# Performance work log

Measured on AMD Instinct MI355X. Metric: run time of the kernel, lower is better.

Reference implementation:

```python
import jax, jax.numpy as jnp
import numpy as np

HEADS = 16
HEAD_DIM = 64
EMBED = HEADS * HEAD_DIM  # 1024
N, L = 4, 4096


def setup_inputs() -> dict:
    key = jax.random.key(0)
    k1, k2, k3, k4, k5, k6, k7, k8 = jax.random.split(key, 8)
    s = 0.02
    return {
        "q": jax.random.normal(k1, (N, L, EMBED), jnp.float32),
        "k": jax.random.normal(k2, (N, L, EMBED), jnp.float32),
        "v": jax.random.normal(k3, (N, L, EMBED), jnp.float32),
        "mask": jnp.ones((N, L, HEADS, HEADS), jnp.int32),
        # torch Linear weights: (out_features, in_features)
        "q_w": jax.random.normal(k4, (HEAD_DIM, HEAD_DIM), jnp.float32) * s,
        "k_w": jax.random.normal(k5, (HEAD_DIM, HEAD_DIM), jnp.float32) * s,
        "v_w": jax.random.normal(k6, (HEAD_DIM, HEAD_DIM), jnp.float32) * s,
        "fc_w": jax.random.normal(k7, (EMBED, EMBED), jnp.float32) * s,
        "fc_b": jax.random.normal(k8, (EMBED,), jnp.float32) * s,
    }


def reference(q, k, v, mask, q_w, k_w, v_w, fc_w, fc_b):
    n, ql = q.shape[0], q.shape[1]
    # reshape to (N, L, H, D) and apply per-head-dim linear projections (x @ W.T)
    q4 = q.reshape(n, ql, HEADS, HEAD_DIM) @ q_w.T
    k4 = k.reshape(n, k.shape[1], HEADS, HEAD_DIM) @ k_w.T
    v4 = v.reshape(n, v.shape[1], HEADS, HEAD_DIM) @ v_w.T
    # Faithful to the original: matmul broadcasts over (N, L), contracting head_dim,
    # so logits are (N, L, H, H) -- attention across heads per token.
    scale = 1.0 / jnp.sqrt(jnp.float32(HEAD_DIM))
    logits = jnp.einsum("nlhd,nlgd->nlhg", q4, k4) * scale
    logits = jnp.where(mask == 0, -jnp.inf, logits)
    weights = jax.nn.softmax(logits, axis=-1)
    out4 = jnp.einsum("nlhg,nlgd->nlhd", weights, v4)  # (N, L, H, D)
    # Faithful scrambled reshape: permute to (N, H, L, D) then flatten to (N, L, H*D)
    out = out4.transpose(0, 2, 1, 3).reshape(n, ql, HEADS * HEAD_DIM)
    return out @ fc_w.T + fc_b
```

## Files before the change

### kernel.cpp

```cpp
#include <hip/hip_runtime.h>
#include <hip/hip_bf16.h>
#include <stdint.h>

#define TOKENS 16384
#define LSEQ 4096
#define WPAD 72
#define NT 4

typedef short bf16x8 __attribute__((ext_vector_type(8)));
typedef float f32x4 __attribute__((ext_vector_type(4)));

typedef __attribute__((address_space(1))) void as1_t;
typedef __attribute__((address_space(3))) void as3_t;

__device__ __forceinline__ unsigned short f2bf(float x) {
  __hip_bfloat16 t = __float2bfloat16(x);
  return *reinterpret_cast<unsigned short*>(&t);
}

__device__ __forceinline__ bf16x8 pack8(float4 a, float4 b) {
  bf16x8 t;
  t[0] = (short)f2bf(a.x); t[1] = (short)f2bf(a.y);
  t[2] = (short)f2bf(a.z); t[3] = (short)f2bf(a.w);
  t[4] = (short)f2bf(b.x); t[5] = (short)f2bf(b.y);
  t[6] = (short)f2bf(b.z); t[7] = (short)f2bf(b.w);
  return t;
}

__device__ __forceinline__ void async16(const void* g, void* lds) {
  __builtin_amdgcn_global_load_lds((as1_t*)const_cast<void*>(g),
                                   (as3_t*)lds, 16, 0, 0);
}

__device__ __forceinline__ float4 aload(const float* p) {
  float4 r;
  asm volatile("global_load_dwordx4 %0, %1, off" : "=v"(r) : "v"(p));
  return r;
}
__device__ __forceinline__ int4 aloadi(const int* p) {
  int4 r;
  asm volatile("global_load_dwordx4 %0, %1, off" : "=v"(r) : "v"(p));
  return r;
}
#define WAITCNT(n) asm volatile("s_waitcnt vmcnt(" #n ")" ::: "memory")
#define SBAR() __builtin_amdgcn_sched_barrier(0)

__global__ __launch_bounds__(256) void cvt_bf16(const float* __restrict__ s,
                                                unsigned short* __restrict__ d,
                                                int n4) {
  int i = blockIdx.x * 256 + threadIdx.x;
  if (i < n4) {
    float4 f = ((const float4*)s)[i];
    union { unsigned short us[4]; uint2 u2; } pk;
    pk.us[0] = f2bf(f.x); pk.us[1] = f2bf(f.y);
    pk.us[2] = f2bf(f.z); pk.us[3] = f2bf(f.w);
    ((uint2*)d)[i] = pk.u2;
  }
}

__global__ __launch_bounds__(1024) void prep_weights(
    const float* __restrict__ qw, const float* __restrict__ kw,
    const float* __restrict__ vw, unsigned short* __restrict__ Mout,
    unsigned short* __restrict__ vwout) {
  __shared__ float ql[4096], kl[4096];
  const int t = threadIdx.x;
  ((float4*)ql)[t] = ((const float4*)qw)[t];
  ((float4*)kl)[t] = ((const float4*)kw)[t];
  {
    float4 f = ((const float4*)vw)[t];
    union { unsigned short us[4]; uint2 u2; } pk;
    pk.us[0] = f2bf(f.x); pk.us[1] = f2bf(f.y);
    pk.us[2] = f2bf(f.z); pk.us[3] = f2bf(f.w);
    ((uint2*)vwout)[t] = pk.u2;
  }
  __syncthreads();
  const int f = t >> 4;
  const int e0 = (t & 15) * 4;
  float acc0 = 0.f, acc1 = 0.f, acc2 = 0.f, acc3 = 0.f;
#pragma unroll 8
  for (int d = 0; d < 64; ++d) {
    const float qv = ql[d * 64 + f];
    const float4 kv = *(const float4*)&kl[d * 64 + e0];
    acc0 += qv * kv.x; acc1 += qv * kv.y; acc2 += qv * kv.z; acc3 += qv * kv.w;
  }
  union { unsigned short us[4]; uint2 u2; } pk;
  pk.us[0] = f2bf(acc0); pk.us[1] = f2bf(acc1);
  pk.us[2] = f2bf(acc2); pk.us[3] = f2bf(acc3);
  *(uint2*)&Mout[f * 64 + e0] = pk.u2;
}

__global__ __launch_bounds__(256) void attn8(
    const float* __restrict__ q, const float* __restrict__ k,
    const float* __restrict__ v, const int* __restrict__ mask,
    const unsigned short* __restrict__ Mg, const unsigned short* __restrict__ vwg,
    unsigned short* __restrict__ X) {
  __shared__ char Mlb[8192];
  __shared__ char Vwb[8192];
  __shared__ char scr_[4][2048];

  const int tid = threadIdx.x;
  const int l = tid & 63, w = tid >> 6;
  const int lr = l & 15, lg = l >> 4;
  char* scr = scr_[w];

#pragma unroll
  for (int i = 0; i < 2; ++i) {
    const int idx = tid + i * 256;
    const int row = idx >> 3, c = idx & 7;
    const int dst = row * 128 + ((c * 16) ^ ((row & 7) << 4));
    *(uint4*)(Mlb + dst) = *(const uint4*)(Mg + row * 64 + c * 8);
    *(uint4*)(Vwb + dst) = *(const uint4*)(vwg + row * 64 + c * 8);
  }
  __syncthreads();

  const int r7 = lr & 7;
  const int wc0 = (lg * 16) ^ (r7 << 4);
  const int wc1 = (64 + lg * 16) ^ (r7 << 4);
  const int fr0 = lr * 128 + ((lg * 16) ^ (r7 << 4));
  const int fr1 = lr * 128 + ((64 + lg * 16) ^ (r7 << 4));
  const int off = lr * 64 + lg * 8;

  const int tok0 = (blockIdx.x * 4 + w) * NT;

  float4 L[12];
  int4 Lm;
  {
    const size_t tb = (size_t)tok0 * 1024;
    L[0] = aload(q + tb + off);      L[1] = aload(q + tb + off + 4);
    L[2] = aload(q + tb + off + 32); L[3] = aload(q + tb + off + 36);
    L[4] = aload(k + tb + off);      L[5] = aload(k + tb + off + 4);
    L[6] = aload(k + tb + off + 32); L[7] = aload(k + tb + off + 36);
    L[8] = aload(v + tb + off);      L[9] = aload(v + tb + off + 4);
    L[10] = aload(v + tb + off + 32); L[11] = aload(v + tb + off + 36);
    Lm = aloadi(mask + (size_t)tok0 * 256 + lr * 16 + lg * 4);
  }

#pragma unroll
  for (int t = 0; t < NT; ++t) {
    const int tok = tok0 + t;

    if (t == 0) { WAITCNT(0); } else { WAITCNT(2); }
    SBAR();

    const bf16x8 aq0 = pack8(L[0], L[1]),  aq1 = pack8(L[2], L[3]);
    const bf16x8 ak0 = pack8(L[4], L[5]),  ak1 = pack8(L[6], L[7]);
    const bf16x8 av0 = pack8(L[8], L[9]),  av1 = pack8(L[10], L[11]);
    const int4 mk4 = Lm;
    SBAR();

    if (t < NT - 1) {
      const size_t tb = (size_t)(tok + 1) * 1024;
      L[0] = aload(q + tb + off);      L[1] = aload(q + tb + off + 4);
      L[2] = aload(q + tb + off + 32); L[3] = aload(q + tb + off + 36);
      L[4] = aload(k + tb + off);      L[5] = aload(k + tb + off + 4);
      L[6] = aload(k + tb + off + 32); L[7] = aload(k + tb + off + 36);
      L[8] = aload(v + tb + off);      L[9] = aload(v + tb + off + 4);
      L[10] = aload(v + tb + off + 32); L[11] = aload(v + tb + off + 36);
      Lm = aloadi(mask + (size_t)(tok + 1) * 256 + lr * 16 + lg * 4);
    }
    SBAR();

    f32x4 accu[4], accv[4];
#pragma unroll
    for (int n = 0; n < 4; ++n) {
      const int wrow = (n * 16 + lr) * 128;
      f32x4 z = {};
      const bf16x8 bm0 = *(const bf16x8*)(Mlb + wrow + wc0);
      const bf16x8 bm1 = *(const bf16x8*)(Mlb + wrow + wc1);
      accu[n] = __builtin_amdgcn_mfma_f32_16x16x32_bf16(ak0, bm0, z, 0, 0, 0);
      accu[n] = __builtin_amdgcn_mfma_f32_16x16x32_bf16(ak1, bm1, accu[n], 0, 0, 0);
      const bf16x8 bw0 = *(const bf16x8*)(Vwb + wrow + wc0);
      const bf16x8 bw1 = *(const bf16x8*)(Vwb + wrow + wc1);
      accv[n] = __builtin_amdgcn_mfma_f32_16x16x32_bf16(av0, bw0, z, 0, 0, 0);
      accv[n] = __builtin_amdgcn_mfma_f32_16x16x32_bf16(av1, bw1, accv[n], 0, 0, 0);
    }

#pragma unroll
    for (int n = 0; n < 4; ++n)
#pragma unroll
      for (int r = 0; r < 4; ++r) {
        const int row = lg * 4 + r;
        *(unsigned short*)(scr + row * 128 + ((32 * n + 2 * lr) ^ ((row & 7) << 4))) =
            f2bf(accu[n][r]);
      }
    const bf16x8 ua0 = *(const bf16x8*)(scr + fr0);
    const bf16x8 ua1 = *(const bf16x8*)(scr + fr1);
    f32x4 z4 = {};
    f32x4 st = __builtin_amdgcn_mfma_f32_16x16x32_bf16(ua0, aq0, z4, 0, 0, 0);
    st = __builtin_amdgcn_mfma_f32_16x16x32_bf16(ua1, aq1, st, 0, 0, 0);

    float e[4];
    float sm = 0.f;
    const int mks[4] = {mk4.x, mk4.y, mk4.z, mk4.w};
#pragma unroll
    for (int r = 0; r < 4; ++r) {
      e[r] = (mks[r] != 0) ? __expf(st[r] * 0.125f) : 0.f;
      sm += e[r];
    }
    sm += __shfl_xor(sm, 16);
    sm += __shfl_xor(sm, 32);
    const float inv = 1.0f / sm;
#pragma unroll
    for (int r = 0; r < 4; ++r) e[r] *= inv;

    bf16x8 apv;
#pragma unroll
    for (int j = 0; j < 8; ++j) {
      const int srcg = (lg * 2 + (j >> 2)) & 3;
      const float pv = __shfl(e[j & 3], lr + srcg * 16, 64);
      apv[j] = (short)((lg < 2) ? f2bf(pv) : (unsigned short)0);
    }

    const int s0 = lr + ((lg & 1) * 2) * 16;
    const int s1 = s0 + 16;
    f32x4 o[4];
#pragma unroll
    for (int n = 0; n < 4; ++n) {
      bf16x8 bv;
#pragma unroll
      for (int j = 0; j < 8; ++j) {
        const float xv = __shfl(accv[n][j & 3], (j < 4) ? s0 : s1, 64);
        bv[j] = (short)f2bf(xv);
      }
      f32x4 z = {};
      o[n] = __builtin_amdgcn_mfma_f32_16x16x32_bf16(apv, bv, z, 0, 0, 0);
    }

#pragma unroll
    for (int n = 0; n < 4; ++n)
#pragma unroll
      for (int r = 0; r < 4; ++r) {
        const int row = lg * 4 + r;
        *(unsigned short*)(scr + row * 128 + ((32 * n + 2 * lr) ^ ((row & 7) << 4))) =
            f2bf(o[n][r]);
      }
    const int nb = tok >> 12, lpos = tok & (LSEQ - 1);
#pragma unroll
    for (int it = 0; it < 2; ++it) {
      const int idx = it * 64 + l;
      const int h = idx >> 3, c = idx & 7;
      const uint4 val = *(const uint4*)(scr + h * 128 + ((c * 16) ^ ((h & 7) << 4)));
      *(uint4*)&X[((size_t)(nb * 16 + h) * LSEQ + lpos) * 64 + c * 8] = val;
    }
  }
}

__global__ __launch_bounds__(256) void gemm_fc(const unsigned short* __restrict__ A,
                                               const unsigned short* __restrict__ B,
                                               const float* __restrict__ bias,
                                               float* __restrict__ C) {
  __shared__ unsigned short sA[128 * 32];
  __shared__ unsigned short sB[128 * 32];
  const int tid = threadIdx.x;
  const int l = tid & 63, w = tid >> 6;
  const int wr = w >> 1, wc = w & 1;

  const int bid = blockIdx.x;
  const int wg = (bid & 7) * 128 + (bid >> 3);
  const int tm = (wg >> 3) * 128;
  const int tn = (wg & 7) * 128;

  f32x4 acc[4][4] = {};

  const int r0 = w * 16 + (l >> 2);
  const int c8 = (l & 3) * 8;

  for (int kt = 0; kt < 32; ++kt) {
    const int k0 = kt * 32;
#pragma unroll
    for (int s = 0; s < 2; ++s) {
      async16(A + (size_t)(tm + s * 64 + r0) * 1024 + k0 + c8,
              (char*)sA + s * 4096 + w * 1024);
      async16(B + (size_t)(tn + s * 64 + r0) * 1024 + k0 + c8,
              (char*)sB + s * 4096 + w * 1024);
    }
    __syncthreads();

    bf16x8 af[4], bfr[4];
#pragma unroll
    for (int fi = 0; fi < 4; ++fi)
      af[fi] = *(const bf16x8*)((const char*)sA +
                                (wr * 64 + fi * 16 + (l & 15)) * 64 + (l >> 4) * 16);
#pragma unroll
    for (int fj = 0; fj < 4; ++fj)
      bfr[fj] = *(const bf16x8*)((const char*)sB +
                                 (wc * 64 + fj * 16 + (l & 15)) * 64 + (l >> 4) * 16);
#pragma unroll
    for (int fi = 0; fi < 4; ++fi)
#pragma unroll
      for (int fj = 0; fj < 4; ++fj)
        acc[fi][fj] = __builtin_amdgcn_mfma_f32_16x16x32_bf16(af[fi], bfr[fj],
                                                              acc[fi][fj], 0, 0, 0);
    __syncthreads();
  }

#pragma unroll
  for (int fj = 0; fj < 4; ++fj) {
    const int col = tn + wc * 64 + fj * 16 + (l & 15);
    const float bv = bias[col];
#pragma unroll
    for (int fi = 0; fi < 4; ++fi) {
#pragma unroll
      for (int r = 0; r < 4; ++r) {
        const int row = tm + wr * 64 + fi * 16 + (l >> 4) * 4 + r;
        C[(size_t)row * 1024 + col] = acc[fi][fj][r] + bv;
      }
    }
  }
}

extern "C" void kernel_launch(void* const* d_in, const int* in_sizes, int n_in,
                              void* d_out, int out_size, void* d_ws, size_t ws_size,
                              hipStream_t stream) {
  (void)in_sizes; (void)n_in; (void)out_size; (void)ws_size;
  const float* q   = (const float*)d_in[0];
  const float* k   = (const float*)d_in[1];
  const float* v   = (const float*)d_in[2];
  const int*  mask = (const int*)d_in[3];
  const float* qw  = (const float*)d_in[4];
  const float* kw  = (const float*)d_in[5];
  const float* vw  = (const float*)d_in[6];
  const float* fcw = (const float*)d_in[7];
  const float* fcb = (const float*)d_in[8];
  float* out = (float*)d_out;

  unsigned short* X   = (unsigned short*)d_ws;
  unsigned short* Wb  = X + (size_t)16 * 1024 * 1024;
  unsigned short* Mw  = Wb + (size_t)1024 * 1024;
  unsigned short* vwb = Mw + 4096;

  cvt_bf16<<<dim3(1024), dim3(256), 0, stream>>>(fcw, Wb, 262144);
  prep_weights<<<dim3(1), dim3(1024), 0, stream>>>(qw, kw, vw, Mw, vwb);
  attn8<<<dim3(1024), dim3(256), 0, stream>>>(q, k, v, mask, Mw, vwb, X);
  gemm_fc<<<dim3(1024), dim3(256), 0, stream>>>(X, Wb, fcb, out);
}
```

Before: 116.1 us.

## Process one token per wave with direct weight loads and LDS V transpose

```diff
diff --git a/kernel.cpp b/kernel.cpp
--- a/kernel.cpp
+++ b/kernel.cpp
@@ -4,8 +4,7 @@
 
 #define TOKENS 16384
 #define LSEQ 4096
-#define WPAD 72
-#define NT 4
+#define VPAD 24
 
 typedef short bf16x8 __attribute__((ext_vector_type(8)));
 typedef float f32x4 __attribute__((ext_vector_type(4)));
@@ -89,159 +88,115 @@
   *(uint2*)&Mout[f * 64 + e0] = pk.u2;
 }
 
-__global__ __launch_bounds__(256) void attn8(
+__global__ __launch_bounds__(256) void attn9(
     const float* __restrict__ q, const float* __restrict__ k,
     const float* __restrict__ v, const int* __restrict__ mask,
     const unsigned short* __restrict__ Mg, const unsigned short* __restrict__ vwg,
     unsigned short* __restrict__ X) {
-  __shared__ char Mlb[8192];
-  __shared__ char Vwb[8192];
   __shared__ char scr_[4][2048];
+  __shared__ unsigned short vt_[4][64 * VPAD];
 
   const int tid = threadIdx.x;
   const int l = tid & 63, w = tid >> 6;
   const int lr = l & 15, lg = l >> 4;
   char* scr = scr_[w];
-
-#pragma unroll
-  for (int i = 0; i < 2; ++i) {
-    const int idx = tid + i * 256;
-    const int row = idx >> 3, c = idx & 7;
-    const int dst = row * 128 + ((c * 16) ^ ((row & 7) << 4));
-    *(uint4*)(Mlb + dst) = *(const uint4*)(Mg + row * 64 + c * 8);
-    *(uint4*)(Vwb + dst) = *(const uint4*)(vwg + row * 64 + c * 8);
-  }
-  __syncthreads();
+  unsigned short* VT = vt_[w];
+
+  const int tok = blockIdx.x * 4 + w;
+  const size_t tb = (size_t)tok * 1024;
+  const int off = lr * 64 + lg * 8;
+
+  float4 L0 = aload(q + tb + off),      L1 = aload(q + tb + off + 4);
+  float4 L2 = aload(q + tb + off + 32), L3 = aload(q + tb + off + 36);
+  float4 L4 = aload(k + tb + off),      L5 = aload(k + tb + off + 4);
+  float4 L6 = aload(k + tb + off + 32), L7 = aload(k + tb + off + 36);
+  float4 L8 = aload(v + tb + off),      L9 = aload(v + tb + off + 4);
+  float4 La = aload(v + tb + off + 32), Lb = aload(v + tb + off + 36);
+  int4 mk4 = aloadi(mask + (size_t)tok * 256 + lr * 16 + lg * 4);
+  WAITCNT(0);
+  SBAR();
+
+  const bf16x8 aq0 = pack8(L0, L1), aq1 = pack8(L2, L3);
+  const bf16x8 ak0 = pack8(L4, L5), ak1 = pack8(L6, L7);
+  const bf16x8 av0 = pack8(L8, L9), av1 = pack8(La, Lb);
+
+  f32x4 accu[4], accv[4];
+#pragma unroll
+  for (int n = 0; n < 4; ++n) {
+    const int wrow = (n * 16 + lr) * 64;
+    f32x4 z = {};
+    const bf16x8 bm0 = *(const bf16x8*)(Mg + wrow + lg * 8);
+    const bf16x8 bm1 = *(const bf16x8*)(Mg + wrow + 32 + lg * 8);
+    accu[n] = __builtin_amdgcn_mfma_f32_16x16x32_bf16(ak0, bm0, z, 0, 0, 0);
+    accu[n] = __builtin_amdgcn_mfma_f32_16x16x32_bf16(ak1, bm1, accu[n], 0, 0, 0);
+    const bf16x8 bw0 = *(const bf16x8*)(vwg + wrow + lg * 8);
+    const bf16x8 bw1 = *(const bf16x8*)(vwg + wrow + 32 + lg * 8);
+    accv[n] = __builtin_amdgcn_mfma_f32_16x16x32_bf16(av0, bw0, z, 0, 0, 0);
+    accv[n] = __builtin_amdgcn_mfma_f32_16x16x32_bf16(av1, bw1, accv[n], 0, 0, 0);
+  }
+
+#pragma unroll
+  for (int n = 0; n < 4; ++n)
+#pragma unroll
+    for (int r = 0; r < 4; ++r) {
+      const int row = lg * 4 + r;
+      *(unsigned short*)(scr + row * 128 + ((32 * n + 2 * lr) ^ ((row & 7) << 4))) =
+          f2bf(accu[n][r]);
+      VT[(n * 16 + lr) * VPAD + lg * 4 + r] = f2bf(accv[n][r]);
+    }
 
   const int r7 = lr & 7;
-  const int wc0 = (lg * 16) ^ (r7 << 4);
-  const int wc1 = (64 + lg * 16) ^ (r7 << 4);
-  const int fr0 = lr * 128 + ((lg * 16) ^ (r7 << 4));
-  const int fr1 = lr * 128 + ((64 + lg * 16) ^ (r7 << 4));
-  const int off = lr * 64 + lg * 8;
-
-  const int tok0 = (blockIdx.x * 4 + w) * NT;
-
-  float4 L[12];
-  int4 Lm;
-  {
-    const size_t tb = (size_t)tok0 * 1024;
-    L[0] = aload(q + tb + off);      L[1] = aload(q + tb + off + 4);
-    L[2] = aload(q + tb + off + 32); L[3] = aload(q + tb + off + 36);
-    L[4] = aload(k + tb + off);      L[5] = aload(k + tb + off + 4);
-    L[6] = aload(k + tb + off + 32); L[7] = aload(k + tb + off + 36);
-    L[8] = aload(v + tb + off);      L[9] = aload(v + tb + off + 4);
-    L[10] = aload(v + tb + off + 32); L[11] = aload(v + tb + off + 36);
-    Lm = aloadi(mask + (size_t)tok0 * 256 + lr * 16 + lg * 4);
-  }
-
-#pragma unroll
-  for (int t = 0; t < NT; ++t) {
-    const int tok = tok0 + t;
-
-    if (t == 0) { WAITCNT(0); } else { WAITCNT(2); }
-    SBAR();
-
-    const bf16x8 aq0 = pack8(L[0], L[1]),  aq1 = pack8(L[2], L[3]);
-    const bf16x8 ak0 = pack8(L[4], L[5]),  ak1 = pack8(L[6], L[7]);
-    const bf16x8 av0 = pack8(L[8], L[9]),  av1 = pack8(L[10], L[11]);
-    const int4 mk4 = Lm;
-    SBAR();
-
-    if (t < NT - 1) {
-      const size_t tb = (size_t)(tok + 1) * 1024;
-      L[0] = aload(q + tb + off);      L[1] = aload(q + tb + off + 4);
-      L[2] = aload(q + tb + off + 32); L[3] = aload(q + tb + off + 36);
-      L[4] = aload(k + tb + off);      L[5] = aload(k + tb + off + 4);
-      L[6] = aload(k + tb + off + 32); L[7] = aload(k + tb + off + 36);
-      L[8] = aload(v + tb + off);      L[9] = aload(v + tb + off + 4);
-      L[10] = aload(v + tb + off + 32); L[11] = aload(v + tb + off + 36);
-      Lm = aloadi(mask + (size_t)(tok + 1) * 256 + lr * 16 + lg * 4);
-    }
-    SBAR();
-
-    f32x4 accu[4], accv[4];
-#pragma unroll
-    for (int n = 0; n < 4; ++n) {
-      const int wrow = (n * 16 + lr) * 128;
-      f32x4 z = {};
-      const bf16x8 bm0 = *(const bf16x8*)(Mlb + wrow + wc0);
-      const bf16x8 bm1 = *(const bf16x8*)(Mlb + wrow + wc1);
-      accu[n] = __builtin_amdgcn_mfma_f32_16x16x32_bf16(ak0, bm0, z, 0, 0, 0);
-      accu[n] = __builtin_amdgcn_mfma_f32_16x16x32_bf16(ak1, bm1, accu[n], 0, 0, 0);
-      const bf16x8 bw0 = *(const bf16x8*)(Vwb + wrow + wc0);
-      const bf16x8 bw1 = *(const bf16x8*)(Vwb + wrow + wc1);
-      accv[n] = __builtin_amdgcn_mfma_f32_16x16x32_bf16(av0, bw0, z, 0, 0, 0);
-      accv[n] = __builtin_amdgcn_mfma_f32_16x16x32_bf16(av1, bw1, accv[n], 0, 0, 0);
-    }
-
-#pragma unroll
-    for (int n = 0; n < 4; ++n)
-#pragma unroll
-      for (int r = 0; r < 4; ++r) {
-        const int row = lg * 4 + r;
-        *(unsigned short*)(scr + row * 128 + ((32 * n + 2 * lr) ^ ((row & 7) << 4))) =
-            f2bf(accu[n][r]);
-      }
-    const bf16x8 ua0 = *(const bf16x8*)(scr + fr0);
-    const bf16x8 ua1 = *(const bf16x8*)(scr + fr1);
-    f32x4 z4 = {};
-    f32x4 st = __builtin_amdgcn_mfma_f32_16x16x32_bf16(ua0, aq0, z4, 0, 0, 0);
-    st = __builtin_amdgcn_mfma_f32_16x16x32_bf16(ua1, aq1, st, 0, 0, 0);
-
-    float e[4];
-    float sm = 0.f;
-    const int mks[4] = {mk4.x, mk4.y, mk4.z, mk4.w};
+  const bf16x8 ua0 = *(const bf16x8*)(scr + lr * 128 + ((lg * 16) ^ (r7 << 4)));
+  const bf16x8 ua1 = *(const bf16x8*)(scr + lr * 128 + ((64 + lg * 16) ^ (r7 << 4)));
+  f32x4 z4 = {};
+  f32x4 st = __builtin_amdgcn_mfma_f32_16x16x32_bf16(ua0, aq0, z4, 0, 0, 0);
+  st = __builtin_amdgcn_mfma_f32_16x16x32_bf16(ua1, aq1, st, 0, 0, 0);
+
+  float e[4];
+  float sm = 0.f;
+  const int mks[4] = {mk4.x, mk4.y, mk4.z, mk4.w};
+#pragma unroll
+  for (int r = 0; r < 4; ++r) {
+    e[r] = (mks[r] != 0) ? __expf(st[r] * 0.125f) : 0.f;
+    sm += e[r];
+  }
+  sm += __shfl_xor(sm, 16);
+  sm += __shfl_xor(sm, 32);
+  const float inv = 1.0f / sm;
+#pragma unroll
+  for (int r = 0; r < 4; ++r) e[r] *= inv;
+
+  bf16x8 apv;
+#pragma unroll
+  for (int j = 0; j < 8; ++j) {
+    const int srcg = (lg * 2 + (j >> 2)) & 3;
+    const float pv = __shfl(e[j & 3], lr + srcg * 16, 64);
+    apv[j] = (short)((lg < 2) ? f2bf(pv) : (unsigned short)0);
+  }
+
+  f32x4 o[4];
+#pragma unroll
+  for (int n = 0; n < 4; ++n) {
+    const bf16x8 bv = *(const bf16x8*)&VT[(n * 16 + lr) * VPAD + (lg & 1) * 8];
+    f32x4 z = {};
+    o[n] = __builtin_amdgcn_mfma_f32_16x16x32_bf16(apv, bv, z, 0, 0, 0);
+  }
+
+#pragma unroll
+  for (int n = 0; n < 4; ++n)
 #pragma unroll
     for (int r = 0; r < 4; ++r) {
-      e[r] = (mks[r] != 0) ? __expf(st[r] * 0.125f) : 0.f;
-      sm += e[r];
-    }
-    sm += __shfl_xor(sm, 16);
-    sm += __shfl_xor(sm, 32);
-    const float inv = 1.0f / sm;
-#pragma unroll
-    for (int r = 0; r < 4; ++r) e[r] *= inv;
-
-    bf16x8 apv;
-#pragma unroll
-    for (int j = 0; j < 8; ++j) {
-      const int srcg = (lg * 2 + (j >> 2)) & 3;
-      const float pv = __shfl(e[j & 3], lr + srcg * 16, 64);
-      apv[j] = (short)((lg < 2) ? f2bf(pv) : (unsigned short)0);
-    }
-
-    const int s0 = lr + ((lg & 1) * 2) * 16;
-    const int s1 = s0 + 16;
-    f32x4 o[4];
-#pragma unroll
-    for (int n = 0; n < 4; ++n) {
-      bf16x8 bv;
-#pragma unroll
-      for (int j = 0; j < 8; ++j) {
-        const float xv = __shfl(accv[n][j & 3], (j < 4) ? s0 : s1, 64);
-        bv[j] = (short)f2bf(xv);
-      }
-      f32x4 z = {};
-      o[n] = __builtin_amdgcn_mfma_f32_16x16x32_bf16(apv, bv, z, 0, 0, 0);
-    }
-
-#pragma unroll
-    for (int n = 0; n < 4; ++n)
-#pragma unroll
-      for (int r = 0; r < 4; ++r) {
-        const int row = lg * 4 + r;
-        *(unsigned short*)(scr + row * 128 + ((32 * n + 2 * lr) ^ ((row & 7) << 4))) =
-            f2bf(o[n][r]);
-      }
-    const int nb = tok >> 12, lpos = tok & (LSEQ - 1);
-#pragma unroll
-    for (int it = 0; it < 2; ++it) {
-      const int idx = it * 64 + l;
-      const int h = idx >> 3, c = idx & 7;
-      const uint4 val = *(const uint4*)(scr + h * 128 + ((c * 16) ^ ((h & 7) << 4)));
-      *(uint4*)&X[((size_t)(nb * 16 + h) * LSEQ + lpos) * 64 + c * 8] = val;
-    }
+      const int row = lg * 4 + r;
+      *(unsigned short*)(scr + row * 128 + ((32 * n + 2 * lr) ^ ((row & 7) << 4))) =
+          f2bf(o[n][r]);
+    }
+  const int nb = tok >> 12, lpos = tok & (LSEQ - 1);
+#pragma unroll
+  for (int it = 0; it < 2; ++it) {
+    const int idx = it * 64 + l;
+    const int h = idx >> 3, c = idx & 7;
+    const uint4 val = *(const uint4*)(scr + h * 128 + ((c * 16) ^ ((h & 7) << 4)));
+    *(uint4*)&X[((size_t)(nb * 16 + h) * LSEQ + lpos) * 64 + c * 8] = val;
   }
 }
 
@@ -331,6 +286,6 @@
 
   cvt_bf16<<<dim3(1024), dim3(256), 0, stream>>>(fcw, Wb, 262144);
   prep_weights<<<dim3(1), dim3(1024), 0, stream>>>(qw, kw, vw, Mw, vwb);
-  attn8<<<dim3(1024), dim3(256), 0, stream>>>(q, k, v, mask, Mw, vwb, X);
+  attn9<<<dim3(4096), dim3(256), 0, stream>>>(q, k, v, mask, Mw, vwb, X);
   gemm_fc<<<dim3(1024), dim3(256), 0, stream>>>(X, Wb, fcb, out);
 }
```

New measurement: 125.7 us. +8.2%, slower.
